# Kernel tuning notes

Hardware: AMD Instinct MI355X
Metric: run time of the kernel (lower is better)

Reference implementation:

```python
import jax, jax.numpy as jnp
import numpy as np

N, E = 50000, 800000
IN = HID = OUT = 128
H, L, EDIM = 4, 3, 3
C = HID // H  # per-head channels = 32
EPS = 1e-5
NEG_SLOPE = 0.2


def setup_inputs() -> dict:
    key = jax.random.key(0)
    ks = jax.random.split(key, 10)

    def p(k, shape, fan_in):
        return jax.random.normal(k, shape, jnp.float32) * (fan_in ** -0.5)

    return {
        "x": jax.random.normal(ks[0], (N, IN), jnp.float32),
        "edge_index": jax.random.randint(ks[1], (2, E), 0, N),
        "edge_attr": jax.random.normal(ks[2], (E, EDIM), jnp.float32),
        # stacked per-layer GATv2 params (layer0 in==hidden so shapes match)
        "Wl": p(ks[3], (L, HID, H * C), HID),   # lin_l (source)
        "Wr": p(ks[4], (L, HID, H * C), HID),   # lin_r (target)
        "We": p(ks[5], (L, EDIM, H * C), EDIM), # lin_edge
        "att": p(ks[6], (L, H, C), C),          # attention vector a
        "ln_w": jnp.ones((L, HID), jnp.float32),
        "ln_b": jnp.zeros((L, HID), jnp.float32),
        "Wout": p(ks[7], (HID, OUT), HID),      # final jk Linear
        "bout": jnp.zeros((OUT,), jnp.float32),
    }


def _gatv2_layer(h, src, dst, edge_attr, Wl, Wr, We, att):
    # h: [N, F]; returns [N, H*C]
    xl = (h @ Wl).reshape(N, H, C)            # source transform
    xr = (h @ Wr).reshape(N, H, C)            # target transform
    ea = (edge_attr @ We).reshape(E, H, C)
    m = xl[src] + xr[dst] + ea                # [E, H, C]
    m = jax.nn.leaky_relu(m, NEG_SLOPE)
    logits = jnp.einsum('ehc,hc->eh', m, att)  # [E, H]
    # segment softmax over incoming edges of each destination node
    lmax = jax.ops.segment_max(logits, dst, num_segments=N)  # [N, H]
    lmax = jnp.where(jnp.isfinite(lmax), lmax, 0.0)
    ex = jnp.exp(logits - lmax[dst])
    denom = jax.ops.segment_sum(ex, dst, num_segments=N)
    alpha = ex / (denom[dst] + 1e-16)          # [E, H]
    msg = xl[src] * alpha[:, :, None]          # [E, H, C]
    out = jax.ops.segment_sum(msg, dst, num_segments=N)
    return out.reshape(N, H * C)


def _graph_layernorm(h, w, b):
    # PyG LayerNorm(mode='graph'): normalize over ALL nodes and features of the graph
    mean = jnp.mean(h)
    var = jnp.mean((h - mean) ** 2)
    return (h - mean) * jax.lax.rsqrt(var + EPS) * w + b


def reference(x, edge_index, edge_attr, Wl, Wr, We, att, ln_w, ln_b, Wout, bout):
    src, dst = edge_index[0], edge_index[1]
    h = x
    for l in range(L):  # small fixed layer loop
        h = _gatv2_layer(h, src, dst, edge_attr, Wl[l], Wr[l], We[l], att[l])
        h = _graph_layernorm(h, ln_w[l], ln_b[l])
        h = jax.nn.gelu(h, approximate=False)
        # dropout = 0.0 -> identity
    return h @ Wout + bout
```

## Files before the change

### kernel.cpp

```cpp
#include <hip/hip_runtime.h>
#include <hip/hip_bf16.h>
#include <math.h>

#define HID 128
#define NHEAD 4
#define CH 32
#define NLAYER 3
#define EDIM 3
#define EPSLN 1e-5f
#define SLOPE 0.2f
#define RSLOTS 1024
#define PAD_W -1e30f
#define LOG2E 1.4426950408889634f

typedef __bf16 bf16x8 __attribute__((ext_vector_type(8)));
typedef float f32x4 __attribute__((ext_vector_type(4)));
typedef float f32x2 __attribute__((ext_vector_type(2)));

__device__ __forceinline__ float bflo(unsigned d) { return __uint_as_float(d << 16); }
__device__ __forceinline__ float bfhi(unsigned d) { return __uint_as_float(d & 0xffff0000u); }

#define DPP_ADD(x, ctrl) \
    (x + __int_as_float(__builtin_amdgcn_update_dpp(0, __float_as_int(x), ctrl, 0xf, 0xf, true)))

__global__ void k_count(const int* __restrict__ dst, int* __restrict__ deg, int E) {
    int i = blockIdx.x * blockDim.x + threadIdx.x;
    if (i < E) atomicAdd(&deg[dst[i]], 1);
}

__global__ __launch_bounds__(1024) void k_scan(const int* __restrict__ deg,
                                               int* __restrict__ outs,
                                               int N, int G) {
    __shared__ int sw[16];
    __shared__ int scarry;
    int tid = threadIdx.x, lane = tid & 63, wid = tid >> 6;
    if (tid == 0) scarry = 0;
    __syncthreads();
    for (int base = 0; base < G; base += 1024) {
        int i = base + tid;
        int v = 0;
        if (i < G) {
            int n0 = 4 * i;
            if (n0 + 3 < N) {
                int4 d4 = *(const int4*)&deg[n0];
                v = ((d4.x + 3) & ~3) + ((d4.y + 3) & ~3) +
                    ((d4.z + 3) & ~3) + ((d4.w + 3) & ~3);
            } else {
#pragma unroll
                for (int j = 0; j < 4; j++) {
                    int n = n0 + j;
                    if (n < N) v += (deg[n] + 3) & ~3;
                }
            }
        }
        int x = v;
#pragma unroll
        for (int o = 1; o < 64; o <<= 1) { int y = __shfl_up(x, o, 64); if (lane >= o) x += y; }
        if (lane == 63) sw[wid] = x;
        __syncthreads();
        int carry = scarry;
        if (tid < 16) {
            int s = sw[tid];
#pragma unroll
            for (int o = 1; o < 16; o <<= 1) { int y = __shfl_up(s, o, 64); if (tid >= o) s += y; }
            sw[tid] = s;
        }
        __syncthreads();
        int wofs = (wid == 0) ? 0 : sw[wid - 1];
        int incl = carry + wofs + x;
        if (i < G) outs[i] = incl - v;
        __syncthreads();
        if (tid == 0) scarry = carry + sw[15];
        __syncthreads();
    }
    if (tid == 0) outs[G] = scarry;
}

__global__ void k_nodepad(const int* __restrict__ deg, const int* __restrict__ groupstart,
                          int* __restrict__ slotbase, int* __restrict__ cursor,
                          int4* __restrict__ slots, int N) {
    int i = blockIdx.x * blockDim.x + threadIdx.x;
    if (i >= N) return;
    int g = i >> 2;
    int base = groupstart[g];
    int i0 = g * 4;
#pragma unroll
    for (int j = 0; j < 3; j++)
        if (i0 + j < i) base += (deg[i0 + j] + 3) & ~3;
    slotbase[i] = base;
    cursor[i] = base;
    int d = deg[i];
    int pd = (d + 3) & ~3;
    for (int j = d; j < pd; j++) slots[base + j] = make_int4(-1, 0, 0, 0);
}

__global__ void k_fill2(const int* __restrict__ src, const int* __restrict__ dst,
                        const float* __restrict__ eattr, int* __restrict__ cursor,
                        int4* __restrict__ slots, int E) {
    int i = blockIdx.x * blockDim.x + threadIdx.x;
    if (i < E) {
        int n = dst[i];
        int slot = atomicAdd(&cursor[n], 1);
        slots[slot] = make_int4(src[i], __float_as_int(eattr[3 * i]),
                                __float_as_int(eattr[3 * i + 1]),
                                __float_as_int(eattr[3 * i + 2]));
    }
}

__global__ __launch_bounds__(256) void k_wprep(const float* __restrict__ Wl,
                                               const float* __restrict__ Wr,
                                               const float* __restrict__ Wout,
                                               __hip_bfloat16* __restrict__ wz) {
    int b = blockIdx.x;
    const float* src = (b < 6) ? ((b & 1) ? Wr + (size_t)(b >> 1) * 16384
                                          : Wl + (size_t)(b >> 1) * 16384)
                               : Wout;
    for (int t = threadIdx.x; t < 16384; t += 256) {
        int j = t & 7, q = (t >> 3) & 63, n = (t >> 9) & 7, s = t >> 12;
        int k = s * 32 + (q >> 4) * 8 + j;
        int c = n * 16 + (q & 15);
        wz[(size_t)b * 16384 + t] = __float2bfloat16(src[k * 128 + c]);
    }
}

__global__ __launch_bounds__(256) void k_cast(const float* __restrict__ in,
                                              __hip_bfloat16* __restrict__ out, int n) {
    int i = (blockIdx.x * 256 + threadIdx.x) * 4;
    if (i < n) {
        float4 v = *(const float4*)&in[i];
        __hip_bfloat16 o[4] = {__float2bfloat16(v.x), __float2bfloat16(v.y),
                               __float2bfloat16(v.z), __float2bfloat16(v.w)};
        *(ushort4*)&out[i] = *(ushort4*)o;
    }
}

template <bool BF16OUT>
__global__ __launch_bounds__(256) void k_gemm_mfma(const __hip_bfloat16* __restrict__ Xb,
                                                   const __hip_bfloat16* __restrict__ Wz0,
                                                   const __hip_bfloat16* __restrict__ Wz1,
                                                   void* __restrict__ Y0v,
                                                   void* __restrict__ Y1v,
                                                   const float* __restrict__ bias, int N) {
    __shared__ __hip_bfloat16 sW[16384];
    const __hip_bfloat16* Wz = blockIdx.y ? Wz1 : Wz0;
    void* Yv = blockIdx.y ? Y1v : Y0v;
    int tid = threadIdx.x;
    {
        const float4* s4 = (const float4*)Wz;
        float4* d4 = (float4*)sW;
#pragma unroll
        for (int i = 0; i < 8; i++) d4[tid + 256 * i] = s4[tid + 256 * i];
    }
    __syncthreads();

    int wv = tid >> 6, lane = tid & 63;
    int quad = lane >> 4, l16 = lane & 15;
    int mbase = blockIdx.x * 128 + wv * 32;

    f32x4 acc[2][8];
#pragma unroll
    for (int mt = 0; mt < 2; mt++)
#pragma unroll
        for (int n = 0; n < 8; n++) acc[mt][n] = (f32x4){0.f, 0.f, 0.f, 0.f};

#pragma unroll
    for (int s = 0; s < 4; s++) {
        bf16x8 a[2];
#pragma unroll
        for (int mt = 0; mt < 2; mt++) {
            int row = mbase + mt * 16 + l16;
            row = (row < N) ? row : (N - 1);
            a[mt] = *(const bf16x8*)&Xb[(size_t)row * HID + s * 32 + quad * 8];
        }
#pragma unroll
        for (int n = 0; n < 8; n++) {
            bf16x8 b = *(const bf16x8*)&sW[((s * 8 + n) * 64 + lane) * 8];
            acc[0][n] = __builtin_amdgcn_mfma_f32_16x16x32_bf16(a[0], b, acc[0][n], 0, 0, 0);
            acc[1][n] = __builtin_amdgcn_mfma_f32_16x16x32_bf16(a[1], b, acc[1][n], 0, 0, 0);
        }
    }

    float bv[8];
#pragma unroll
    for (int n = 0; n < 8; n++) bv[n] = bias ? bias[n * 16 + l16] : 0.f;

#pragma unroll
    for (int mt = 0; mt < 2; mt++)
#pragma unroll
        for (int reg = 0; reg < 4; reg++) {
            int row = mbase + mt * 16 + quad * 4 + reg;
            if (row < N) {
                if (BF16OUT) {
                    __hip_bfloat16* yp = (__hip_bfloat16*)Yv + (size_t)row * HID + l16;
#pragma unroll
                    for (int n = 0; n < 8; n++) yp[n * 16] = __float2bfloat16(acc[mt][n][reg]);
                } else {
                    float* yp = (float*)Yv + (size_t)row * HID + l16;
#pragma unroll
                    for (int n = 0; n < 8; n++) yp[n * 16] = acc[mt][n][reg] + bv[n];
                }
            }
        }
}

__global__ __launch_bounds__(256) void k_aggregate(const __hip_bfloat16* __restrict__ xlb,
                                                   const __hip_bfloat16* __restrict__ xrb,
                                                   const int4* __restrict__ slots,
                                                   const int* __restrict__ deg,
                                                   const int* __restrict__ slotbase,
                                                   const float* __restrict__ We,
                                                   const float* __restrict__ att,
                                                   unsigned* __restrict__ tmpp,
                                                   float* __restrict__ red, int N) {
    int wid = threadIdx.x >> 6;
    int lane = threadIdx.x & 63;
    int node = blockIdx.x * 4 + wid;
    if (node >= N) return;
    int c0 = lane * 2;
    int head = lane >> 4;

    f32x2 we0, we1, we2;
    { float2 t = *(const float2*)&We[c0];            we0 = (f32x2){t.x, t.y}; }
    { float2 t = *(const float2*)&We[HID + c0];      we1 = (f32x2){t.x, t.y}; }
    { float2 t = *(const float2*)&We[2 * HID + c0];  we2 = (f32x2){t.x, t.y}; }
    float at0 = att[head * CH + (c0 & 31)] * LOG2E;
    float at1 = att[head * CH + (c0 & 31) + 1] * LOG2E;

    int base = __builtin_amdgcn_readfirstlane(slotbase[node]);
    int steps = __builtin_amdgcn_readfirstlane((deg[node] + 3) >> 2);

    unsigned dxr = *(const unsigned*)&xrb[(size_t)node * HID + c0];
    f32x2 xr2 = (f32x2){bflo(dxr), bfhi(dxr)};

    float l = 0.f;
    f32x2 Av = (f32x2){0.f, 0.f};

    const int4* vp = slots + base;

    for (int t = 0; t < steps; t++) {
        int4 v[4];
#pragma unroll
        for (int j = 0; j < 4; j++) v[j] = vp[4 * t + j];
        unsigned dv[4];
#pragma unroll
        for (int j = 0; j < 4; j++) {
            int si = max(v[j].x, 0);
            dv[j] = *(const unsigned*)&xlb[(size_t)si * HID + c0];
        }
#pragma unroll
        for (int j = 0; j < 4; j++) {
            float e0 = __int_as_float(v[j].y);
            float e1 = __int_as_float(v[j].z);
            float e2 = __int_as_float(v[j].w);
            float padw = (v[j].x < 0) ? PAD_W : 0.f;
            f32x2 xv = (f32x2){bflo(dv[j]), bfhi(dv[j])};
            f32x2 m = __builtin_elementwise_fma(we2, (f32x2)e2, xv + xr2);
            m = __builtin_elementwise_fma(we1, (f32x2)e1, m);
            m = __builtin_elementwise_fma(we0, (f32x2)e0, m);
            f32x2 ms = m * SLOPE;
            m.x = fmaxf(m.x, ms.x);
            m.y = fmaxf(m.y, ms.y);
            float part = fmaf(m.x, at0, m.y * at1);
            part = DPP_ADD(part, 0xB1);
            part = DPP_ADD(part, 0x4E);
            part = DPP_ADD(part, 0x141);
            part = DPP_ADD(part, 0x140);
            float p = __builtin_amdgcn_exp2f(part + padw);
            l += p;
            Av = __builtin_elementwise_fma((f32x2)p, xv, Av);
        }
    }

    float inv = 1.f / (l + 1e-16f);
    f32x2 o2 = Av * inv;
    __hip_bfloat16 pk[2] = {__float2bfloat16(o2.x), __float2bfloat16(o2.y)};
    tmpp[(size_t)node * (HID / 2) + lane] = *(unsigned*)pk;

    float ssum = o2.x + o2.y;
    float ssq = fmaf(o2.x, o2.x, o2.y * o2.y);
#pragma unroll
    for (int o = 32; o >= 1; o >>= 1) { ssum += __shfl_xor(ssum, o); ssq += __shfl_xor(ssq, o); }
    if (lane == 0) {
        int slot = (node & (RSLOTS - 1)) * 2;
        atomicAdd(&red[slot], ssum);
        atomicAdd(&red[slot + 1], ssq);
    }
}

__global__ __launch_bounds__(256) void k_ln_gelu(const uint4* __restrict__ in4,
                                                 const float* __restrict__ w,
                                                 const float* __restrict__ b,
                                                 const float* __restrict__ red,
                                                 float M,
                                                 uint4* __restrict__ out4, int n8) {
    __shared__ float ls[8];
    int tid = threadIdx.x;
    float s = 0.f, q = 0.f;
    const float2* r2 = (const float2*)red;
    for (int i = tid; i < RSLOTS; i += 256) { float2 rv = r2[i]; s += rv.x; q += rv.y; }
#pragma unroll
    for (int o = 32; o >= 1; o >>= 1) { s += __shfl_xor(s, o); q += __shfl_xor(q, o); }
    if ((tid & 63) == 0) { ls[(tid >> 6) * 2] = s; ls[(tid >> 6) * 2 + 1] = q; }
    __syncthreads();
    float S = ls[0] + ls[2] + ls[4] + ls[6];
    float Q = ls[1] + ls[3] + ls[5] + ls[7];
    float mean = S / M;
    float inv = rsqrtf(Q / M - mean * mean + EPSLN);

    int i = blockIdx.x * blockDim.x + tid;
    if (i >= n8) return;
    uint4 v = in4[i];
    int col = (i * 8) & 127;
    float4 w0 = *(const float4*)&w[col], w1 = *(const float4*)&w[col + 4];
    float4 b0 = *(const float4*)&b[col], b1 = *(const float4*)&b[col + 4];
    float r[8] = {bflo(v.x), bfhi(v.x), bflo(v.y), bfhi(v.y),
                  bflo(v.z), bfhi(v.z), bflo(v.w), bfhi(v.w)};
    float wr[8] = {w0.x, w0.y, w0.z, w0.w, w1.x, w1.y, w1.z, w1.w};
    float br[8] = {b0.x, b0.y, b0.z, b0.w, b1.x, b1.y, b1.z, b1.w};
    __hip_bfloat16 o[8];
#pragma unroll
    for (int j = 0; j < 8; j++) {
        float t = fmaf((r[j] - mean) * inv, wr[j], br[j]);
        o[j] = __float2bfloat16(0.5f * t * (1.f + erff(t * 0.70710678118654752f)));
    }
    out4[i] = *(uint4*)o;
}

extern "C" void kernel_launch(void* const* d_in, const int* in_sizes, int n_in,
                              void* d_out, int out_size, void* d_ws, size_t ws_size,
                              hipStream_t stream) {
    const float* x = (const float*)d_in[0];
    const int* ei = (const int*)d_in[1];
    const float* eattr = (const float*)d_in[2];
    const float* Wl = (const float*)d_in[3];
    const float* Wr = (const float*)d_in[4];
    const float* We = (const float*)d_in[5];
    const float* att = (const float*)d_in[6];
    const float* lnw = (const float*)d_in[7];
    const float* lnb = (const float*)d_in[8];
    const float* Wout = (const float*)d_in[9];
    const float* bout = (const float*)d_in[10];
    float* out = (float*)d_out;

    int N = in_sizes[0] / HID;
    int E = in_sizes[1] / 2;
    int G = (N + 3) / 4;
    int SCAP = E + 8 * N;
    const int* src = ei;
    const int* dst = ei + E;

    char* w = (char*)d_ws;
    __hip_bfloat16* hb = (__hip_bfloat16*)w;   w += (size_t)N * HID * 2;
    __hip_bfloat16* xlb = (__hip_bfloat16*)w;  w += (size_t)N * HID * 2;
    __hip_bfloat16* xrb = (__hip_bfloat16*)w;  w += (size_t)N * HID * 2;
    unsigned* tmpp = (unsigned*)w;             w += (size_t)N * HID * 2;
    __hip_bfloat16* wz = (__hip_bfloat16*)w;   w += (size_t)7 * 16384 * 2;
    int4* slots = (int4*)w;       w += (size_t)SCAP * 16;
    int* deg = (int*)w;           w += (size_t)N * 4;
    int* cursor = (int*)w;        w += (size_t)N * 4;
    float* red = (float*)w;       w += (size_t)NLAYER * RSLOTS * 2 * 4;
    int* slotbase = (int*)w;      w += (size_t)N * 4;
    int* groupstart = (int*)w;    w += (size_t)(G + 1) * 4;

    hipMemsetAsync(deg, 0, (size_t)(2 * N + NLAYER * RSLOTS * 2) * 4, stream);
    k_count<<<(E + 255) / 256, 256, 0, stream>>>(dst, deg, E);
    k_scan<<<1, 1024, 0, stream>>>(deg, groupstart, N, G);
    k_nodepad<<<(N + 255) / 256, 256, 0, stream>>>(deg, groupstart, slotbase, cursor, slots, N);
    k_fill2<<<(E + 255) / 256, 256, 0, stream>>>(src, dst, eattr, cursor, slots, E);
    k_wprep<<<7, 256, 0, stream>>>(Wl, Wr, Wout, wz);
    k_cast<<<(N * HID / 4 + 255) / 256, 256, 0, stream>>>(x, hb, N * HID);

    int gb = (N + 127) / 128;
    float M = (float)N * (float)HID;
    for (int l = 0; l < NLAYER; l++) {
        float* redl = red + (size_t)l * RSLOTS * 2;
        k_gemm_mfma<true><<<dim3(gb, 2), 256, 0, stream>>>(
            hb, wz + (size_t)(2 * l) * 16384, wz + (size_t)(2 * l + 1) * 16384,
            xlb, xrb, nullptr, N);
        k_aggregate<<<(N + 3) / 4, 256, 0, stream>>>(
            xlb, xrb, slots, deg, slotbase,
            We + (size_t)l * EDIM * HID, att + (size_t)l * NHEAD * CH, tmpp, redl, N);
        k_ln_gelu<<<((N * HID / 8) + 255) / 256, 256, 0, stream>>>(
            (const uint4*)tmpp, lnw + (size_t)l * HID, lnb + (size_t)l * HID, redl, M,
            (uint4*)hb, N * HID / 8);
    }
    k_gemm_mfma<false><<<dim3(gb, 1), 256, 0, stream>>>(
        hb, wz + (size_t)6 * 16384, wz + (size_t)6 * 16384, out, out, bout, N);
}
```

Before: 438.2 us.

## Split wavefront into four edge groups with 8 channels per lane in aggregation

The aggregation kernel now splits each 64-lane wavefront into four 16-lane groups. Each group handles a different edge of every 4-edge step, and each lane covers 8 channels using 16-byte loads instead of 2 channels per lane. The per-head dot product now needs only two DPP steps, and the partial softmax sums and accumulators are merged across groups with shuffles at the end. This cuts per-edge instruction count and widens the gather loads, at the cost of more registers and a final cross-group reduction.

```diff
diff --git a/kernel.cpp b/kernel.cpp
--- a/kernel.cpp
+++ b/kernel.cpp
@@ -216,68 +216,109 @@
     int lane = threadIdx.x & 63;
     int node = blockIdx.x * 4 + wid;
     if (node >= N) return;
-    int c0 = lane * 2;
-    int head = lane >> 4;
-
-    f32x2 we0, we1, we2;
-    { float2 t = *(const float2*)&We[c0];            we0 = (f32x2){t.x, t.y}; }
-    { float2 t = *(const float2*)&We[HID + c0];      we1 = (f32x2){t.x, t.y}; }
-    { float2 t = *(const float2*)&We[2 * HID + c0];  we2 = (f32x2){t.x, t.y}; }
-    float at0 = att[head * CH + (c0 & 31)] * LOG2E;
-    float at1 = att[head * CH + (c0 & 31) + 1] * LOG2E;
+    int grp = lane >> 4;
+    int q = lane & 15;
+    int head = q >> 2;
+    int cb = q * 8;
+
+    f32x2 we0[4], we1[4], we2[4], at[4];
+    {
+        float4 a = *(const float4*)&We[cb], b = *(const float4*)&We[cb + 4];
+        we0[0] = (f32x2){a.x, a.y}; we0[1] = (f32x2){a.z, a.w};
+        we0[2] = (f32x2){b.x, b.y}; we0[3] = (f32x2){b.z, b.w};
+    }
+    {
+        float4 a = *(const float4*)&We[HID + cb], b = *(const float4*)&We[HID + cb + 4];
+        we1[0] = (f32x2){a.x, a.y}; we1[1] = (f32x2){a.z, a.w};
+        we1[2] = (f32x2){b.x, b.y}; we1[3] = (f32x2){b.z, b.w};
+    }
+    {
+        float4 a = *(const float4*)&We[2 * HID + cb], b = *(const float4*)&We[2 * HID + cb + 4];
+        we2[0] = (f32x2){a.x, a.y}; we2[1] = (f32x2){a.z, a.w};
+        we2[2] = (f32x2){b.x, b.y}; we2[3] = (f32x2){b.z, b.w};
+    }
+    {
+        int ab = head * CH + (cb & 31);
+        float4 a = *(const float4*)&att[ab], b = *(const float4*)&att[ab + 4];
+        at[0] = (f32x2){a.x * LOG2E, a.y * LOG2E}; at[1] = (f32x2){a.z * LOG2E, a.w * LOG2E};
+        at[2] = (f32x2){b.x * LOG2E, b.y * LOG2E}; at[3] = (f32x2){b.z * LOG2E, b.w * LOG2E};
+    }
 
     int base = __builtin_amdgcn_readfirstlane(slotbase[node]);
     int steps = __builtin_amdgcn_readfirstlane((deg[node] + 3) >> 2);
 
-    unsigned dxr = *(const unsigned*)&xrb[(size_t)node * HID + c0];
-    f32x2 xr2 = (f32x2){bflo(dxr), bfhi(dxr)};
+    f32x2 xr[4];
+    {
+        uint4 rx = *(const uint4*)&xrb[(size_t)node * HID + cb];
+        xr[0] = (f32x2){bflo(rx.x), bfhi(rx.x)};
+        xr[1] = (f32x2){bflo(rx.y), bfhi(rx.y)};
+        xr[2] = (f32x2){bflo(rx.z), bfhi(rx.z)};
+        xr[3] = (f32x2){bflo(rx.w), bfhi(rx.w)};
+    }
 
     float l = 0.f;
-    f32x2 Av = (f32x2){0.f, 0.f};
-
-    const int4* vp = slots + base;
+    f32x2 A[4];
+#pragma unroll
+    for (int k = 0; k < 4; k++) A[k] = (f32x2){0.f, 0.f};
+
+    const int4* vp = slots + base + grp;
 
     for (int t = 0; t < steps; t++) {
-        int4 v[4];
-#pragma unroll
-        for (int j = 0; j < 4; j++) v[j] = vp[4 * t + j];
-        unsigned dv[4];
-#pragma unroll
-        for (int j = 0; j < 4; j++) {
-            int si = max(v[j].x, 0);
-            dv[j] = *(const unsigned*)&xlb[(size_t)si * HID + c0];
-        }
-#pragma unroll
-        for (int j = 0; j < 4; j++) {
-            float e0 = __int_as_float(v[j].y);
-            float e1 = __int_as_float(v[j].z);
-            float e2 = __int_as_float(v[j].w);
-            float padw = (v[j].x < 0) ? PAD_W : 0.f;
-            f32x2 xv = (f32x2){bflo(dv[j]), bfhi(dv[j])};
-            f32x2 m = __builtin_elementwise_fma(we2, (f32x2)e2, xv + xr2);
-            m = __builtin_elementwise_fma(we1, (f32x2)e1, m);
-            m = __builtin_elementwise_fma(we0, (f32x2)e0, m);
-            f32x2 ms = m * SLOPE;
-            m.x = fmaxf(m.x, ms.x);
-            m.y = fmaxf(m.y, ms.y);
-            float part = fmaf(m.x, at0, m.y * at1);
-            part = DPP_ADD(part, 0xB1);
-            part = DPP_ADD(part, 0x4E);
-            part = DPP_ADD(part, 0x141);
-            part = DPP_ADD(part, 0x140);
-            float p = __builtin_amdgcn_exp2f(part + padw);
-            l += p;
-            Av = __builtin_elementwise_fma((f32x2)p, xv, Av);
-        }
+        int4 v = vp[4 * t];
+        int si = max(v.x, 0);
+        uint4 dx = *(const uint4*)&xlb[(size_t)si * HID + cb];
+        float e0 = __int_as_float(v.y);
+        float e1 = __int_as_float(v.z);
+        float e2 = __int_as_float(v.w);
+        float padw = (v.x < 0) ? PAD_W : 0.f;
+        f32x2 xv[4];
+        xv[0] = (f32x2){bflo(dx.x), bfhi(dx.x)};
+        xv[1] = (f32x2){bflo(dx.y), bfhi(dx.y)};
+        xv[2] = (f32x2){bflo(dx.z), bfhi(dx.z)};
+        xv[3] = (f32x2){bflo(dx.w), bfhi(dx.w)};
+        f32x2 dot = (f32x2){0.f, 0.f};
+#pragma unroll
+        for (int k = 0; k < 4; k++) {
+            f32x2 m = __builtin_elementwise_fma(we2[k], (f32x2)e2, xv[k] + xr[k]);
+            m = __builtin_elementwise_fma(we1[k], (f32x2)e1, m);
+            m = __builtin_elementwise_fma(we0[k], (f32x2)e0, m);
+            m = __builtin_elementwise_max(m, m * SLOPE);
+            dot = __builtin_elementwise_fma(m, at[k], dot);
+        }
+        float part = dot.x + dot.y;
+        part = DPP_ADD(part, 0xB1);
+        part = DPP_ADD(part, 0x4E);
+        float p = __builtin_amdgcn_exp2f(part + padw);
+        l += p;
+#pragma unroll
+        for (int k = 0; k < 4; k++) A[k] = __builtin_elementwise_fma((f32x2)p, xv[k], A[k]);
+    }
+
+    l += __shfl_xor(l, 16);
+    l += __shfl_xor(l, 32);
+#pragma unroll
+    for (int k = 0; k < 4; k++) {
+        A[k].x += __shfl_xor(A[k].x, 16);
+        A[k].y += __shfl_xor(A[k].y, 16);
+        A[k].x += __shfl_xor(A[k].x, 32);
+        A[k].y += __shfl_xor(A[k].y, 32);
     }
 
     float inv = 1.f / (l + 1e-16f);
-    f32x2 o2 = Av * inv;
-    __hip_bfloat16 pk[2] = {__float2bfloat16(o2.x), __float2bfloat16(o2.y)};
-    tmpp[(size_t)node * (HID / 2) + lane] = *(unsigned*)pk;
-
-    float ssum = o2.x + o2.y;
-    float ssq = fmaf(o2.x, o2.x, o2.y * o2.y);
+    float ssum = 0.f, ssq = 0.f;
+    if (grp == 0) {
+        unsigned pk[4];
+#pragma unroll
+        for (int k = 0; k < 4; k++) {
+            f32x2 o2 = A[k] * inv;
+            __hip_bfloat16 h[2] = {__float2bfloat16(o2.x), __float2bfloat16(o2.y)};
+            pk[k] = *(unsigned*)h;
+            ssum += o2.x + o2.y;
+            ssq += fmaf(o2.x, o2.x, o2.y * o2.y);
+        }
+        *(uint4*)&tmpp[(size_t)node * (HID / 2) + q * 4] =
+            make_uint4(pk[0], pk[1], pk[2], pk[3]);
+    }
 #pragma unroll
     for (int o = 32; o >= 1; o >>= 1) { ssum += __shfl_xor(ssum, o); ssq += __shfl_xor(ssq, o); }
     if (lane == 0) {
```

New measurement: 493.7 us. 12.7% more time.
